# Performance work log

Hardware: AMD Instinct MI355X
Metric: run time of the kernel (lower is better)

## Reference

```python
import jax, jax.numpy as jnp
import numpy as np

B, N, T, S = 32, 102400, 64, 1600
PI = float(np.pi)
EPS = 1e-12  # numerical guard inside sqrt for cdist (diagonal is exactly 0)


def _cdist(a, b):
    # a: (..., P, 3), b: (..., Q, 3) -> (..., P, Q) euclidean distances
    sq = jnp.sum((a[..., :, None, :] - b[..., None, :, :]) ** 2, axis=-1)
    return jnp.sqrt(sq + EPS)


def _rigid_t(alpha, trans, sz, center):
    # alpha, trans: (B, T, 3). Returns XYZ (B,T,3,3), translation (B,T,3).
    c, s = jnp.cos(alpha), jnp.sin(alpha)
    z = jnp.zeros_like(c[..., 0]); o = jnp.ones_like(c[..., 0])
    X = jnp.stack([c[..., 0], -s[..., 0], z, s[..., 0], c[..., 0], z, z, z, o], -1).reshape(*alpha.shape[:2], 3, 3)
    Y = jnp.stack([c[..., 1], z, s[..., 1], z, o, z, -s[..., 1], z, c[..., 1]], -1).reshape(*alpha.shape[:2], 3, 3)
    Z = jnp.stack([o, z, z, z, c[..., 2], -s[..., 2], z, s[..., 2], c[..., 2]], -1).reshape(*alpha.shape[:2], 3, 3)
    XYZ = jnp.einsum('btij,btjk,btkl->btil', X, Y, Z)
    eye = jnp.eye(3, dtype=alpha.dtype)
    Tt = trans * sz[None, None, :] + jnp.einsum('m,btmk->btk', center, eye[None, None] - XYZ)
    return XYZ, Tt


def setup_inputs():
    key = jax.random.key(0)
    ks = jax.random.split(key, 6)
    x = jax.random.normal(ks[0], (B, 6, N), jnp.float32)
    w1 = jax.random.normal(ks[1], (3 * N, 32), jnp.float32) * 0.005
    b1 = jnp.zeros((32,), jnp.float32)
    w2 = jax.random.normal(ks[2], (32, 6 * T), jnp.float32) * 0.05
    b2 = jnp.zeros((6 * T,), jnp.float32)
    A = jax.random.normal(ks[3], (6, N), jnp.float32)
    mask = jax.random.uniform(ks[4], (T, T), jnp.float32)
    sz = jnp.array([128.0, 128.0, 64.0], jnp.float32)
    tess = jnp.arange(N, dtype=jnp.int32).reshape(T, S)  # equal-size partition
    return {'x': x, 'w1': w1, 'b1': b1, 'w2': w2, 'b2': b2, 'A': A, 'mask': mask, 'sz': sz, 'tess': tess}


def reference(x, w1, b1, w2, b2, A, mask, sz, tess):
    center = sz / 2.0
    # localization MLP on flattened xyz coords: (B, 3N) -> (B, T, 6)
    xflat = x[:, :3, :].reshape(B, 3 * N)
    h = jax.nn.relu(xflat @ w1 + b1)
    z_l = jnp.tanh(h @ w2 + b2).reshape(B, T, 6)
    # NOTE: original code uses z_l[:, :, 3:] for BOTH angles and translation
    r_, t_ = _rigid_t(PI * z_l[:, :, 3:], z_l[:, :, 3:], sz, center)
    x3 = x[:, :3, :]
    xg = x3[:, :, tess]  # gather: (B, 3, T, S)
    # out[b,j,p,n] = sum_k r_[b,p,k,j] * xg[b,k,p,n]  (matches einsum 'bkt,bkn->btn')
    rot = jnp.einsum('bpkj,bkpn->bjpn', r_, xg) + t_.transpose(0, 2, 1)[:, :, :, None]
    # scatter back into full point cloud (tess partitions N)
    X3 = jnp.zeros_like(x3).at[:, :, tess.reshape(-1)].set(rot.reshape(B, 3, N))
    X_t = jnp.concatenate([X3, x[:, 3:, :]], axis=1)  # colors pass through identity
    # regularizer on per-piece centroids
    pts_1 = A[:3][:, tess].mean(axis=2).T                 # (T, 3)
    pts_2 = X3[:, :, tess].mean(axis=3).transpose(0, 2, 1)  # (B, T, 3)
    diff = _cdist(pts_1, pts_1)[None] - _cdist(pts_2, pts_2)
    reg = jnp.sum((mask[None] * diff) ** 2, axis=(1, 2))  # (B,)
    return X_t, reg
```

## Files before the change

kernel.cpp:

```cpp
#include <hip/hip_runtime.h>
#include <hip/hip_bf16.h>
#include <math.h>

#define BB 32
#define NN 102400
#define TT 64
#define SS 1600
#define K3N (3 * NN)
#define KC 64
#define G1 512
#define NCHUNK (K3N / KC)
#define XP 68
#define WP 40
#define PI_F 3.14159265358979323846f

__global__ __launch_bounds__(256) void k1_gemm(const float* __restrict__ x,
                                               const float* __restrict__ w1,
                                               float* __restrict__ h_part) {
    __shared__ float xs[2][32 * XP];
    __shared__ float ws1[2][KC * WP];
    const int tid = threadIdx.x;
    const int ks = tid & 7;
    const int tile = tid >> 3;
    const int bg = tile & 7;
    const int cg = tile >> 3;
    const int sxb = tid >> 4, sxk = (tid & 15) * 4;
    const int swr = tid >> 3, swc = (tid & 7) * 4;

    float acc[4][8];
    #pragma unroll
    for (int j = 0; j < 4; ++j)
        #pragma unroll
        for (int c = 0; c < 8; ++c) acc[j][c] = 0.f;

    const int start = (int)(((long)blockIdx.x * NCHUNK) / G1);
    const int end   = (int)(((long)(blockIdx.x + 1) * NCHUNK) / G1);

    float4 rx0, rx1, rw0, rw1;
    {
        const int k0 = start * KC;
        rx0 = *(const float4*)(x + (size_t)sxb * 6 * NN + k0 + sxk);
        rx1 = *(const float4*)(x + (size_t)(sxb + 16) * 6 * NN + k0 + sxk);
        rw0 = *(const float4*)(w1 + (size_t)(k0 + swr) * 32 + swc);
        rw1 = *(const float4*)(w1 + (size_t)(k0 + swr + 32) * 32 + swc);
        *(float4*)(xs[0] + sxb * XP + sxk) = rx0;
        *(float4*)(xs[0] + (sxb + 16) * XP + sxk) = rx1;
        *(float4*)(ws1[0] + swr * WP + swc) = rw0;
        *(float4*)(ws1[0] + (swr + 32) * WP + swc) = rw1;
    }
    __syncthreads();

    int cur = 0;
    for (int chunk = start; chunk < end; ++chunk) {
        const bool more = (chunk + 1) < end;
        if (more) {
            const int k0 = (chunk + 1) * KC;
            rx0 = *(const float4*)(x + (size_t)sxb * 6 * NN + k0 + sxk);
            rx1 = *(const float4*)(x + (size_t)(sxb + 16) * 6 * NN + k0 + sxk);
            rw0 = *(const float4*)(w1 + (size_t)(k0 + swr) * 32 + swc);
            rw1 = *(const float4*)(w1 + (size_t)(k0 + swr + 32) * 32 + swc);
        }
        const float* xc = xs[cur];
        const float* wc = ws1[cur];
        #pragma unroll
        for (int i = 0; i < 8; ++i) {
            const int k = ks + 8 * i;
            const float4 wa = *(const float4*)(wc + k * WP + cg * 8);
            const float4 wb = *(const float4*)(wc + k * WP + cg * 8 + 4);
            float xv[4];
            #pragma unroll
            for (int j = 0; j < 4; ++j) xv[j] = xc[(bg + 8 * j) * XP + k];
            #pragma unroll
            for (int j = 0; j < 4; ++j) {
                acc[j][0] = fmaf(xv[j], wa.x, acc[j][0]);
                acc[j][1] = fmaf(xv[j], wa.y, acc[j][1]);
                acc[j][2] = fmaf(xv[j], wa.z, acc[j][2]);
                acc[j][3] = fmaf(xv[j], wa.w, acc[j][3]);
                acc[j][4] = fmaf(xv[j], wb.x, acc[j][4]);
                acc[j][5] = fmaf(xv[j], wb.y, acc[j][5]);
                acc[j][6] = fmaf(xv[j], wb.z, acc[j][6]);
                acc[j][7] = fmaf(xv[j], wb.w, acc[j][7]);
            }
        }
        if (more) {
            const int nb = cur ^ 1;
            *(float4*)(xs[nb] + sxb * XP + sxk) = rx0;
            *(float4*)(xs[nb] + (sxb + 16) * XP + sxk) = rx1;
            *(float4*)(ws1[nb] + swr * WP + swc) = rw0;
            *(float4*)(ws1[nb] + (swr + 32) * WP + swc) = rw1;
        }
        __syncthreads();
        cur ^= 1;
    }

    #pragma unroll
    for (int off = 1; off < 8; off <<= 1) {
        #pragma unroll
        for (int j = 0; j < 4; ++j)
            #pragma unroll
            for (int c = 0; c < 8; ++c)
                acc[j][c] += __shfl_xor(acc[j][c], off, 64);
    }
    if (ks == 0) {
        float* hp = h_part + (size_t)blockIdx.x * 1024;
        #pragma unroll
        for (int j = 0; j < 4; ++j) {
            const int b = bg + 8 * j;
            #pragma unroll
            for (int c = 0; c < 8; ++c)
                hp[b * 32 + cg * 8 + c] = acc[j][c];
        }
    }
}

__global__ __launch_bounds__(256) void kb_fused(const float* __restrict__ h_part,
                                                const float* __restrict__ b1,
                                                const float* __restrict__ w2,
                                                const float* __restrict__ b2,
                                                const float* __restrict__ sz,
                                                const float* __restrict__ A,
                                                const int* __restrict__ tess,
                                                float* __restrict__ RT,
                                                float* __restrict__ pts1) {
    const int blk = blockIdx.x;
    if (blk < BB) {
        const int bb = blk;
        __shared__ float part[8][32];
        __shared__ float hsh[32];
        const int c = threadIdx.x & 31, g = threadIdx.x >> 5;
        float s = 0.f;
        for (int j = g; j < G1; j += 8) s += h_part[(size_t)j * 1024 + bb * 32 + c];
        part[g][c] = s;
        __syncthreads();
        if (threadIdx.x < 32) {
            float acc = 0.f;
            #pragma unroll
            for (int g2 = 0; g2 < 8; ++g2) acc += part[g2][threadIdx.x];
            hsh[threadIdx.x] = fmaxf(acc + b1[threadIdx.x], 0.f);
        }
        __syncthreads();
        const int t = threadIdx.x;
        if (t < TT) {
            float z[3];
            #pragma unroll
            for (int j = 0; j < 3; ++j) {
                const int col = 6 * t + 3 + j;
                float s2 = b2[col];
                #pragma unroll 8
                for (int cc = 0; cc < 32; ++cc) s2 = fmaf(hsh[cc], w2[cc * 384 + col], s2);
                z[j] = tanhf(s2);
            }
            float c0, s0, c1, s1, c2, s2v;
            sincosf(PI_F * z[0], &s0, &c0);
            sincosf(PI_F * z[1], &s1, &c1);
            sincosf(PI_F * z[2], &s2v, &c2);
            const float R00 = c0 * c1;
            const float R01 = -s0 * c2 + c0 * s1 * s2v;
            const float R02 = s0 * s2v + c0 * s1 * c2;
            const float R10 = s0 * c1;
            const float R11 = c0 * c2 + s0 * s1 * s2v;
            const float R12 = -c0 * s2v + s0 * s1 * c2;
            const float R20 = -s1;
            const float R21 = c1 * s2v;
            const float R22 = c1 * c2;
            const float szx = sz[0], szy = sz[1], szz = sz[2];
            const float cx = 0.5f * szx, cy = 0.5f * szy, cz = 0.5f * szz;
            const float T0 = z[0] * szx + cx - (cx * R00 + cy * R10 + cz * R20);
            const float T1 = z[1] * szy + cy - (cx * R01 + cy * R11 + cz * R21);
            const float T2 = z[2] * szz + cz - (cx * R02 + cy * R12 + cz * R22);
            float* o = RT + (bb * TT + t) * 12;
            o[0] = R00; o[1] = R10; o[2]  = R20; o[3]  = T0;
            o[4] = R01; o[5] = R11; o[6]  = R21; o[7]  = T1;
            o[8] = R02; o[9] = R12; o[10] = R22; o[11] = T2;
        }
    } else {
        const int t = blk - BB;
        const int* tr = tess + t * SS;
        float s0 = 0.f, s1 = 0.f, s2 = 0.f;
        for (int s = threadIdx.x; s < SS; s += 256) {
            const int idx = tr[s];
            s0 += A[idx]; s1 += A[NN + idx]; s2 += A[2 * NN + idx];
        }
        #pragma unroll
        for (int o = 32; o > 0; o >>= 1) {
            s0 += __shfl_down(s0, o, 64);
            s1 += __shfl_down(s1, o, 64);
            s2 += __shfl_down(s2, o, 64);
        }
        __shared__ float red[4 * 3];
        const int lane = threadIdx.x & 63, wv = threadIdx.x >> 6;
        if (lane == 0) { red[wv * 3] = s0; red[wv * 3 + 1] = s1; red[wv * 3 + 2] = s2; }
        __syncthreads();
        if (threadIdx.x < 3) {
            const float s = red[threadIdx.x] + red[3 + threadIdx.x] + red[6 + threadIdx.x] + red[9 + threadIdx.x];
            pts1[t * 3 + threadIdx.x] = s * (1.0f / SS);
        }
    }
}

__global__ __launch_bounds__(256) void k3_transform(const float* __restrict__ x,
                                                    const int* __restrict__ tess,
                                                    const float* __restrict__ RT,
                                                    float* __restrict__ out,
                                                    float* __restrict__ pts2) {
    const int blk = blockIdx.x;
    const int b = blk / TT, t = blk % TT;
    const float* p = RT + blk * 12;
    const float M00 = p[0], M01 = p[1], M02 = p[2], T0 = p[3];
    const float M10 = p[4], M11 = p[5], M12 = p[6], T1 = p[7];
    const float M20 = p[8], M21 = p[9], M22 = p[10], T2 = p[11];
    const float* xb = x + (size_t)b * 6 * NN;
    float* ob = out + (size_t)b * 6 * NN;
    const int* tr = tess + t * SS;
    float s0 = 0.f, s1 = 0.f, s2 = 0.f;
    for (int s = threadIdx.x; s < SS; s += 256) {
        const int idx = tr[s];
        const float x0 = xb[idx], x1 = xb[NN + idx], x2 = xb[2 * NN + idx];
        const float y0 = fmaf(M00, x0, fmaf(M01, x1, fmaf(M02, x2, T0)));
        const float y1 = fmaf(M10, x0, fmaf(M11, x1, fmaf(M12, x2, T1)));
        const float y2 = fmaf(M20, x0, fmaf(M21, x1, fmaf(M22, x2, T2)));
        ob[idx] = y0; ob[NN + idx] = y1; ob[2 * NN + idx] = y2;
        s0 += y0; s1 += y1; s2 += y2;
    }
    const int n0 = t * SS;
    for (int i = threadIdx.x; i < 1200; i += 256) {
        const int ch = i / 400, r = i - ch * 400;
        const size_t off = (size_t)(3 + ch) * NN + n0 + r * 4;
        *(float4*)(ob + off) = *(const float4*)(xb + off);
    }
    #pragma unroll
    for (int o = 32; o > 0; o >>= 1) {
        s0 += __shfl_down(s0, o, 64);
        s1 += __shfl_down(s1, o, 64);
        s2 += __shfl_down(s2, o, 64);
    }
    __shared__ float red[4 * 3];
    const int lane = threadIdx.x & 63, wv = threadIdx.x >> 6;
    if (lane == 0) { red[wv * 3] = s0; red[wv * 3 + 1] = s1; red[wv * 3 + 2] = s2; }
    __syncthreads();
    if (threadIdx.x < 3) {
        const float s = red[threadIdx.x] + red[3 + threadIdx.x] + red[6 + threadIdx.x] + red[9 + threadIdx.x];
        pts2[blk * 3 + threadIdx.x] = s * (1.0f / SS);
    }
}

__global__ __launch_bounds__(256) void k5_reg(const float* __restrict__ pts1,
                                              const float* __restrict__ pts2,
                                              const float* __restrict__ mask,
                                              float* __restrict__ out) {
    const int b = blockIdx.x;
    __shared__ float p1[TT * 3], p2[TT * 3];
    for (int i = threadIdx.x; i < TT * 3; i += 256) {
        p1[i] = pts1[i];
        p2[i] = pts2[b * TT * 3 + i];
    }
    __syncthreads();
    float acc = 0.f;
    for (int pr = threadIdx.x; pr < TT * TT; pr += 256) {
        const int t = pr >> 6, u = pr & 63;
        float dx = p1[t * 3] - p1[u * 3];
        float dy = p1[t * 3 + 1] - p1[u * 3 + 1];
        float dz = p1[t * 3 + 2] - p1[u * 3 + 2];
        const float d1 = sqrtf(dx * dx + dy * dy + dz * dz + 1e-12f);
        dx = p2[t * 3] - p2[u * 3];
        dy = p2[t * 3 + 1] - p2[u * 3 + 1];
        dz = p2[t * 3 + 2] - p2[u * 3 + 2];
        const float d2 = sqrtf(dx * dx + dy * dy + dz * dz + 1e-12f);
        const float d = mask[pr] * (d1 - d2);
        acc = fmaf(d, d, acc);
    }
    #pragma unroll
    for (int o = 32; o > 0; o >>= 1) acc += __shfl_down(acc, o, 64);
    __shared__ float red[4];
    const int lane = threadIdx.x & 63, wv = threadIdx.x >> 6;
    if (lane == 0) red[wv] = acc;
    __syncthreads();
    if (threadIdx.x == 0) {
        out[(size_t)BB * 6 * NN + b] = red[0] + red[1] + red[2] + red[3];
    }
}

extern "C" void kernel_launch(void* const* d_in, const int* in_sizes, int n_in,
                              void* d_out, int out_size, void* d_ws, size_t ws_size,
                              hipStream_t stream) {
    const float* x    = (const float*)d_in[0];
    const float* w1   = (const float*)d_in[1];
    const float* b1   = (const float*)d_in[2];
    const float* w2   = (const float*)d_in[3];
    const float* b2   = (const float*)d_in[4];
    const float* A    = (const float*)d_in[5];
    const float* mask = (const float*)d_in[6];
    const float* sz   = (const float*)d_in[7];
    const int*   tess = (const int*)d_in[8];
    float* out = (float*)d_out;
    float* ws  = (float*)d_ws;

    float* h_part = ws;
    float* RT     = h_part + (size_t)G1 * 1024;
    float* pts2   = RT + BB * TT * 12;
    float* pts1   = pts2 + BB * TT * 3;

    k1_gemm<<<G1, 256, 0, stream>>>(x, w1, h_part);
    kb_fused<<<BB + TT, 256, 0, stream>>>(h_part, b1, w2, b2, sz, A, tess, RT, pts1);
    k3_transform<<<BB * TT, 256, 0, stream>>>(x, tess, RT, out, pts2);
    k5_reg<<<BB, 256, 0, stream>>>(pts1, pts2, mask, out);
}
```

Before: 76.77 us.

## Restructure split-K GEMM thread mapping with float4 LDS reads and more blocks

The first GEMM kernel now gives each wave its own contiguous 8-wide K slice and reads x from shared memory as float4 vectors. The cross-lane shuffle reduction is replaced by one shuffle plus a shared-memory reduction across waves. The grid size becomes a runtime value, defaulting to 1024 blocks and capped by workspace size, with launch bounds requesting 4 blocks per CU. This is meant to cut LDS instruction count and shuffle overhead and to raise parallelism. In exchange the second kernel must reduce twice as many partial sums.

```diff
diff --git a/kernel.cpp b/kernel.cpp
--- a/kernel.cpp
+++ b/kernel.cpp
@@ -8,20 +8,20 @@
 #define SS 1600
 #define K3N (3 * NN)
 #define KC 64
-#define G1 512
 #define NCHUNK (K3N / KC)
 #define XP 68
 #define WP 40
 #define PI_F 3.14159265358979323846f
 
-__global__ __launch_bounds__(256) void k1_gemm(const float* __restrict__ x,
-                                               const float* __restrict__ w1,
-                                               float* __restrict__ h_part) {
+__global__ __launch_bounds__(256, 4) void k1_gemm(const float* __restrict__ x,
+                                                  const float* __restrict__ w1,
+                                                  float* __restrict__ h_part,
+                                                  int g1) {
     __shared__ float xs[2][32 * XP];
     __shared__ float ws1[2][KC * WP];
     const int tid = threadIdx.x;
-    const int ks = tid & 7;
-    const int tile = tid >> 3;
+    const int ks = tid >> 5;
+    const int tile = tid & 31;
     const int bg = tile & 7;
     const int cg = tile >> 3;
     const int sxb = tid >> 4, sxk = (tid & 15) * 4;
@@ -33,8 +33,8 @@
         #pragma unroll
         for (int c = 0; c < 8; ++c) acc[j][c] = 0.f;
 
-    const int start = (int)(((long)blockIdx.x * NCHUNK) / G1);
-    const int end   = (int)(((long)(blockIdx.x + 1) * NCHUNK) / G1);
+    const int start = (int)(((long)blockIdx.x * NCHUNK) / g1);
+    const int end   = (int)(((long)(blockIdx.x + 1) * NCHUNK) / g1);
 
     float4 rx0, rx1, rw0, rw1;
     {
@@ -63,23 +63,28 @@
         const float* xc = xs[cur];
         const float* wc = ws1[cur];
         #pragma unroll
-        for (int i = 0; i < 8; ++i) {
-            const int k = ks + 8 * i;
-            const float4 wa = *(const float4*)(wc + k * WP + cg * 8);
-            const float4 wb = *(const float4*)(wc + k * WP + cg * 8 + 4);
-            float xv[4];
-            #pragma unroll
-            for (int j = 0; j < 4; ++j) xv[j] = xc[(bg + 8 * j) * XP + k];
-            #pragma unroll
-            for (int j = 0; j < 4; ++j) {
-                acc[j][0] = fmaf(xv[j], wa.x, acc[j][0]);
-                acc[j][1] = fmaf(xv[j], wa.y, acc[j][1]);
-                acc[j][2] = fmaf(xv[j], wa.z, acc[j][2]);
-                acc[j][3] = fmaf(xv[j], wa.w, acc[j][3]);
-                acc[j][4] = fmaf(xv[j], wb.x, acc[j][4]);
-                acc[j][5] = fmaf(xv[j], wb.y, acc[j][5]);
-                acc[j][6] = fmaf(xv[j], wb.z, acc[j][6]);
-                acc[j][7] = fmaf(xv[j], wb.w, acc[j][7]);
+        for (int i = 0; i < 2; ++i) {
+            const int kb0 = ks * 8 + i * 4;
+            float4 xv[4];
+            #pragma unroll
+            for (int j = 0; j < 4; ++j)
+                xv[j] = *(const float4*)(xc + (bg + 8 * j) * XP + kb0);
+            #pragma unroll
+            for (int kk = 0; kk < 4; ++kk) {
+                const float4 wa = *(const float4*)(wc + (kb0 + kk) * WP + cg * 8);
+                const float4 wb = *(const float4*)(wc + (kb0 + kk) * WP + cg * 8 + 4);
+                #pragma unroll
+                for (int j = 0; j < 4; ++j) {
+                    const float xj = kk == 0 ? xv[j].x : (kk == 1 ? xv[j].y : (kk == 2 ? xv[j].z : xv[j].w));
+                    acc[j][0] = fmaf(xj, wa.x, acc[j][0]);
+                    acc[j][1] = fmaf(xj, wa.y, acc[j][1]);
+                    acc[j][2] = fmaf(xj, wa.z, acc[j][2]);
+                    acc[j][3] = fmaf(xj, wa.w, acc[j][3]);
+                    acc[j][4] = fmaf(xj, wb.x, acc[j][4]);
+                    acc[j][5] = fmaf(xj, wb.y, acc[j][5]);
+                    acc[j][6] = fmaf(xj, wb.z, acc[j][6]);
+                    acc[j][7] = fmaf(xj, wb.w, acc[j][7]);
+                }
             }
         }
         if (more) {
@@ -94,21 +99,44 @@
     }
 
     #pragma unroll
-    for (int off = 1; off < 8; off <<= 1) {
-        #pragma unroll
-        for (int j = 0; j < 4; ++j)
-            #pragma unroll
-            for (int c = 0; c < 8; ++c)
-                acc[j][c] += __shfl_xor(acc[j][c], off, 64);
-    }
-    if (ks == 0) {
+    for (int j = 0; j < 4; ++j)
+        #pragma unroll
+        for (int c = 0; c < 8; ++c)
+            acc[j][c] += __shfl_xor(acc[j][c], 32, 64);
+
+    float* red = &xs[0][0];
+    const int wv = tid >> 6, lane = tid & 63;
+    if (wv > 0 && lane < 32) {
+        float* dst = red + (wv - 1) * 1152 + tile * 36;
+        #pragma unroll
+        for (int j = 0; j < 4; ++j) {
+            float4 v0; v0.x = acc[j][0]; v0.y = acc[j][1]; v0.z = acc[j][2]; v0.w = acc[j][3];
+            float4 v1; v1.x = acc[j][4]; v1.y = acc[j][5]; v1.z = acc[j][6]; v1.w = acc[j][7];
+            *(float4*)(dst + j * 8) = v0;
+            *(float4*)(dst + j * 8 + 4) = v1;
+        }
+    }
+    __syncthreads();
+    if (wv == 0 && lane < 32) {
+        #pragma unroll
+        for (int w2 = 0; w2 < 3; ++w2) {
+            const float* srcp = red + w2 * 1152 + tile * 36;
+            #pragma unroll
+            for (int j = 0; j < 4; ++j) {
+                const float4 v0 = *(const float4*)(srcp + j * 8);
+                const float4 v1 = *(const float4*)(srcp + j * 8 + 4);
+                acc[j][0] += v0.x; acc[j][1] += v0.y; acc[j][2] += v0.z; acc[j][3] += v0.w;
+                acc[j][4] += v1.x; acc[j][5] += v1.y; acc[j][6] += v1.z; acc[j][7] += v1.w;
+            }
+        }
         float* hp = h_part + (size_t)blockIdx.x * 1024;
         #pragma unroll
         for (int j = 0; j < 4; ++j) {
-            const int b = bg + 8 * j;
-            #pragma unroll
-            for (int c = 0; c < 8; ++c)
-                hp[b * 32 + cg * 8 + c] = acc[j][c];
+            float4 v0; v0.x = acc[j][0]; v0.y = acc[j][1]; v0.z = acc[j][2]; v0.w = acc[j][3];
+            float4 v1; v1.x = acc[j][4]; v1.y = acc[j][5]; v1.z = acc[j][6]; v1.w = acc[j][7];
+            float* dst = hp + (bg + 8 * j) * 32 + cg * 8;
+            *(float4*)(dst) = v0;
+            *(float4*)(dst + 4) = v1;
         }
     }
 }
@@ -121,7 +149,8 @@
                                                 const float* __restrict__ A,
                                                 const int* __restrict__ tess,
                                                 float* __restrict__ RT,
-                                                float* __restrict__ pts1) {
+                                                float* __restrict__ pts1,
+                                                int g1) {
     const int blk = blockIdx.x;
     if (blk < BB) {
         const int bb = blk;
@@ -129,7 +158,7 @@
         __shared__ float hsh[32];
         const int c = threadIdx.x & 31, g = threadIdx.x >> 5;
         float s = 0.f;
-        for (int j = g; j < G1; j += 8) s += h_part[(size_t)j * 1024 + bb * 32 + c];
+        for (int j = g; j < g1; j += 8) s += h_part[(size_t)j * 1024 + bb * 32 + c];
         part[g][c] = s;
         __syncthreads();
         if (threadIdx.x < 32) {
@@ -295,13 +324,16 @@
     float* out = (float*)d_out;
     float* ws  = (float*)d_ws;
 
+    int g1 = 1024;
+    while ((size_t)((size_t)g1 * 1024 + 2048 * 12 + 2048 * 3 + 192) * 4 > ws_size && g1 > 128) g1 >>= 1;
+
     float* h_part = ws;
-    float* RT     = h_part + (size_t)G1 * 1024;
+    float* RT     = h_part + (size_t)g1 * 1024;
     float* pts2   = RT + BB * TT * 12;
     float* pts1   = pts2 + BB * TT * 3;
 
-    k1_gemm<<<G1, 256, 0, stream>>>(x, w1, h_part);
-    kb_fused<<<BB + TT, 256, 0, stream>>>(h_part, b1, w2, b2, sz, A, tess, RT, pts1);
+    k1_gemm<<<g1, 256, 0, stream>>>(x, w1, h_part, g1);
+    kb_fused<<<BB + TT, 256, 0, stream>>>(h_part, b1, w2, b2, sz, A, tess, RT, pts1, g1);
     k3_transform<<<BB * TT, 256, 0, stream>>>(x, tess, RT, out, pts2);
     k5_reg<<<BB, 256, 0, stream>>>(pts1, pts2, mask, out);
 }
```

Measured after the change: 140.1 us. +82.5%, slower.

## Overlap color passthrough copy and centroid reduction with the GEMM kernel

Applied to the files above, without the earlier changes.

Extra blocks are added to the first-layer GEMM launch: one group copies the color channels from input to output, and another computes the reference centroids pts1. Both jobs move out of the later kernels, so the bandwidth-bound copy runs while the GEMM reads x and w1 and no longer sits on the dependent transform path. The rigid-transform kernel now only builds rotations. Both jobs now compete with the GEMM for bandwidth, and the copy becomes a grid-stride loop instead of per-tile copies.

```diff
diff --git a/kernel.cpp b/kernel.cpp
--- a/kernel.cpp
+++ b/kernel.cpp
@@ -9,192 +9,201 @@
 #define K3N (3 * NN)
 #define KC 64
 #define G1 512
+#define CPB 512
 #define NCHUNK (K3N / KC)
 #define XP 68
 #define WP 40
 #define PI_F 3.14159265358979323846f
 
-__global__ __launch_bounds__(256) void k1_gemm(const float* __restrict__ x,
+__global__ __launch_bounds__(256) void k1_mega(const float* __restrict__ x,
                                                const float* __restrict__ w1,
-                                               float* __restrict__ h_part) {
-    __shared__ float xs[2][32 * XP];
-    __shared__ float ws1[2][KC * WP];
+                                               const float* __restrict__ A,
+                                               const int* __restrict__ tess,
+                                               float* __restrict__ h_part,
+                                               float* __restrict__ out,
+                                               float* __restrict__ pts1) {
     const int tid = threadIdx.x;
-    const int ks = tid & 7;
-    const int tile = tid >> 3;
-    const int bg = tile & 7;
-    const int cg = tile >> 3;
-    const int sxb = tid >> 4, sxk = (tid & 15) * 4;
-    const int swr = tid >> 3, swc = (tid & 7) * 4;
-
-    float acc[4][8];
-    #pragma unroll
-    for (int j = 0; j < 4; ++j)
-        #pragma unroll
-        for (int c = 0; c < 8; ++c) acc[j][c] = 0.f;
-
-    const int start = (int)(((long)blockIdx.x * NCHUNK) / G1);
-    const int end   = (int)(((long)(blockIdx.x + 1) * NCHUNK) / G1);
-
-    float4 rx0, rx1, rw0, rw1;
-    {
-        const int k0 = start * KC;
-        rx0 = *(const float4*)(x + (size_t)sxb * 6 * NN + k0 + sxk);
-        rx1 = *(const float4*)(x + (size_t)(sxb + 16) * 6 * NN + k0 + sxk);
-        rw0 = *(const float4*)(w1 + (size_t)(k0 + swr) * 32 + swc);
-        rw1 = *(const float4*)(w1 + (size_t)(k0 + swr + 32) * 32 + swc);
-        *(float4*)(xs[0] + sxb * XP + sxk) = rx0;
-        *(float4*)(xs[0] + (sxb + 16) * XP + sxk) = rx1;
-        *(float4*)(ws1[0] + swr * WP + swc) = rw0;
-        *(float4*)(ws1[0] + (swr + 32) * WP + swc) = rw1;
-    }
-    __syncthreads();
-
-    int cur = 0;
-    for (int chunk = start; chunk < end; ++chunk) {
-        const bool more = (chunk + 1) < end;
-        if (more) {
-            const int k0 = (chunk + 1) * KC;
+    if (blockIdx.x < G1) {
+        __shared__ float xs[2][32 * XP];
+        __shared__ float ws1[2][KC * WP];
+        const int ks = tid & 7;
+        const int tile = tid >> 3;
+        const int bg = tile & 7;
+        const int cg = tile >> 3;
+        const int sxb = tid >> 4, sxk = (tid & 15) * 4;
+        const int swr = tid >> 3, swc = (tid & 7) * 4;
+
+        float acc[4][8];
+        #pragma unroll
+        for (int j = 0; j < 4; ++j)
+            #pragma unroll
+            for (int c = 0; c < 8; ++c) acc[j][c] = 0.f;
+
+        const int start = (int)(((long)blockIdx.x * NCHUNK) / G1);
+        const int end   = (int)(((long)(blockIdx.x + 1) * NCHUNK) / G1);
+
+        float4 rx0, rx1, rw0, rw1;
+        {
+            const int k0 = start * KC;
             rx0 = *(const float4*)(x + (size_t)sxb * 6 * NN + k0 + sxk);
             rx1 = *(const float4*)(x + (size_t)(sxb + 16) * 6 * NN + k0 + sxk);
             rw0 = *(const float4*)(w1 + (size_t)(k0 + swr) * 32 + swc);
             rw1 = *(const float4*)(w1 + (size_t)(k0 + swr + 32) * 32 + swc);
-        }
-        const float* xc = xs[cur];
-        const float* wc = ws1[cur];
-        #pragma unroll
-        for (int i = 0; i < 8; ++i) {
-            const int k = ks + 8 * i;
-            const float4 wa = *(const float4*)(wc + k * WP + cg * 8);
-            const float4 wb = *(const float4*)(wc + k * WP + cg * 8 + 4);
-            float xv[4];
+            *(float4*)(xs[0] + sxb * XP + sxk) = rx0;
+            *(float4*)(xs[0] + (sxb + 16) * XP + sxk) = rx1;
+            *(float4*)(ws1[0] + swr * WP + swc) = rw0;
+            *(float4*)(ws1[0] + (swr + 32) * WP + swc) = rw1;
+        }
+        __syncthreads();
+
+        int cur = 0;
+        for (int chunk = start; chunk < end; ++chunk) {
+            const bool more = (chunk + 1) < end;
+            if (more) {
+                const int k0 = (chunk + 1) * KC;
+                rx0 = *(const float4*)(x + (size_t)sxb * 6 * NN + k0 + sxk);
+                rx1 = *(const float4*)(x + (size_t)(sxb + 16) * 6 * NN + k0 + sxk);
+                rw0 = *(const float4*)(w1 + (size_t)(k0 + swr) * 32 + swc);
+                rw1 = *(const float4*)(w1 + (size_t)(k0 + swr + 32) * 32 + swc);
+            }
+            const float* xc = xs[cur];
+            const float* wc = ws1[cur];
             #pragma unroll
-            for (int j = 0; j < 4; ++j) xv[j] = xc[(bg + 8 * j) * XP + k];
+            for (int i = 0; i < 8; ++i) {
+                const int k = ks + 8 * i;
+                const float4 wa = *(const float4*)(wc + k * WP + cg * 8);
+                const float4 wb = *(const float4*)(wc + k * WP + cg * 8 + 4);
+                float xv[4];
+                #pragma unroll
+                for (int j = 0; j < 4; ++j) xv[j] = xc[(bg + 8 * j) * XP + k];
+                #pragma unroll
+                for (int j = 0; j < 4; ++j) {
+                    acc[j][0] = fmaf(xv[j], wa.x, acc[j][0]);
+                    acc[j][1] = fmaf(xv[j], wa.y, acc[j][1]);
+                    acc[j][2] = fmaf(xv[j], wa.z, acc[j][2]);
+                    acc[j][3] = fmaf(xv[j], wa.w, acc[j][3]);
+                    acc[j][4] = fmaf(xv[j], wb.x, acc[j][4]);
+                    acc[j][5] = fmaf(xv[j], wb.y, acc[j][5]);
+                    acc[j][6] = fmaf(xv[j], wb.z, acc[j][6]);
+                    acc[j][7] = fmaf(xv[j], wb.w, acc[j][7]);
+                }
+            }
+            if (more) {
+                const int nb = cur ^ 1;
+                *(float4*)(xs[nb] + sxb * XP + sxk) = rx0;
+                *(float4*)(xs[nb] + (sxb + 16) * XP + sxk) = rx1;
+                *(float4*)(ws1[nb] + swr * WP + swc) = rw0;
+                *(float4*)(ws1[nb] + (swr + 32) * WP + swc) = rw1;
+            }
+            __syncthreads();
+            cur ^= 1;
+        }
+
+        #pragma unroll
+        for (int off = 1; off < 8; off <<= 1) {
+            #pragma unroll
+            for (int j = 0; j < 4; ++j)
+                #pragma unroll
+                for (int c = 0; c < 8; ++c)
+                    acc[j][c] += __shfl_xor(acc[j][c], off, 64);
+        }
+        if (ks == 0) {
+            float* hp = h_part + (size_t)blockIdx.x * 1024;
             #pragma unroll
             for (int j = 0; j < 4; ++j) {
-                acc[j][0] = fmaf(xv[j], wa.x, acc[j][0]);
-                acc[j][1] = fmaf(xv[j], wa.y, acc[j][1]);
-                acc[j][2] = fmaf(xv[j], wa.z, acc[j][2]);
-                acc[j][3] = fmaf(xv[j], wa.w, acc[j][3]);
-                acc[j][4] = fmaf(xv[j], wb.x, acc[j][4]);
-                acc[j][5] = fmaf(xv[j], wb.y, acc[j][5]);
-                acc[j][6] = fmaf(xv[j], wb.z, acc[j][6]);
-                acc[j][7] = fmaf(xv[j], wb.w, acc[j][7]);
+                const int b = bg + 8 * j;
+                #pragma unroll
+                for (int c = 0; c < 8; ++c)
+                    hp[b * 32 + cg * 8 + c] = acc[j][c];
             }
         }
-        if (more) {
-            const int nb = cur ^ 1;
-            *(float4*)(xs[nb] + sxb * XP + sxk) = rx0;
-            *(float4*)(xs[nb] + (sxb + 16) * XP + sxk) = rx1;
-            *(float4*)(ws1[nb] + swr * WP + swc) = rw0;
-            *(float4*)(ws1[nb] + (swr + 32) * WP + swc) = rw1;
-        }
+    } else if (blockIdx.x < G1 + CPB) {
+        const int cb = blockIdx.x - G1;
+        for (long i = (long)cb * 256 + tid; i < 2457600L; i += (long)CPB * 256) {
+            const int b = (int)(i / 76800);
+            const int rem = (int)(i - (long)b * 76800);
+            const size_t off = (size_t)b * (6 * NN) + K3N + (size_t)rem * 4;
+            *(float4*)(out + off) = *(const float4*)(x + off);
+        }
+    } else {
+        const int t = blockIdx.x - G1 - CPB;
+        const int* tr = tess + t * SS;
+        float s0 = 0.f, s1 = 0.f, s2 = 0.f;
+        for (int s = tid; s < SS; s += 256) {
+            const int idx = tr[s];
+            s0 += A[idx]; s1 += A[NN + idx]; s2 += A[2 * NN + idx];
+        }
+        #pragma unroll
+        for (int o = 32; o > 0; o >>= 1) {
+            s0 += __shfl_down(s0, o, 64);
+            s1 += __shfl_down(s1, o, 64);
+            s2 += __shfl_down(s2, o, 64);
+        }
+        __shared__ float red[4 * 3];
+        const int lane = tid & 63, wv = tid >> 6;
+        if (lane == 0) { red[wv * 3] = s0; red[wv * 3 + 1] = s1; red[wv * 3 + 2] = s2; }
         __syncthreads();
-        cur ^= 1;
-    }
-
-    #pragma unroll
-    for (int off = 1; off < 8; off <<= 1) {
-        #pragma unroll
-        for (int j = 0; j < 4; ++j)
-            #pragma unroll
-            for (int c = 0; c < 8; ++c)
-                acc[j][c] += __shfl_xor(acc[j][c], off, 64);
-    }
-    if (ks == 0) {
-        float* hp = h_part + (size_t)blockIdx.x * 1024;
-        #pragma unroll
-        for (int j = 0; j < 4; ++j) {
-            const int b = bg + 8 * j;
-            #pragma unroll
-            for (int c = 0; c < 8; ++c)
-                hp[b * 32 + cg * 8 + c] = acc[j][c];
-        }
-    }
-}
-
-__global__ __launch_bounds__(256) void kb_fused(const float* __restrict__ h_part,
+        if (tid < 3) {
+            const float s = red[tid] + red[3 + tid] + red[6 + tid] + red[9 + tid];
+            pts1[t * 3 + tid] = s * (1.0f / SS);
+        }
+    }
+}
+
+__global__ __launch_bounds__(256) void kb_rigid(const float* __restrict__ h_part,
                                                 const float* __restrict__ b1,
                                                 const float* __restrict__ w2,
                                                 const float* __restrict__ b2,
                                                 const float* __restrict__ sz,
-                                                const float* __restrict__ A,
-                                                const int* __restrict__ tess,
-                                                float* __restrict__ RT,
-                                                float* __restrict__ pts1) {
-    const int blk = blockIdx.x;
-    if (blk < BB) {
-        const int bb = blk;
-        __shared__ float part[8][32];
-        __shared__ float hsh[32];
-        const int c = threadIdx.x & 31, g = threadIdx.x >> 5;
-        float s = 0.f;
-        for (int j = g; j < G1; j += 8) s += h_part[(size_t)j * 1024 + bb * 32 + c];
-        part[g][c] = s;
-        __syncthreads();
-        if (threadIdx.x < 32) {
-            float acc = 0.f;
-            #pragma unroll
-            for (int g2 = 0; g2 < 8; ++g2) acc += part[g2][threadIdx.x];
-            hsh[threadIdx.x] = fmaxf(acc + b1[threadIdx.x], 0.f);
-        }
-        __syncthreads();
-        const int t = threadIdx.x;
-        if (t < TT) {
-            float z[3];
-            #pragma unroll
-            for (int j = 0; j < 3; ++j) {
-                const int col = 6 * t + 3 + j;
-                float s2 = b2[col];
-                #pragma unroll 8
-                for (int cc = 0; cc < 32; ++cc) s2 = fmaf(hsh[cc], w2[cc * 384 + col], s2);
-                z[j] = tanhf(s2);
-            }
-            float c0, s0, c1, s1, c2, s2v;
-            sincosf(PI_F * z[0], &s0, &c0);
-            sincosf(PI_F * z[1], &s1, &c1);
-            sincosf(PI_F * z[2], &s2v, &c2);
-            const float R00 = c0 * c1;
-            const float R01 = -s0 * c2 + c0 * s1 * s2v;
-            const float R02 = s0 * s2v + c0 * s1 * c2;
-            const float R10 = s0 * c1;
-            const float R11 = c0 * c2 + s0 * s1 * s2v;
-            const float R12 = -c0 * s2v + s0 * s1 * c2;
-            const float R20 = -s1;
-            const float R21 = c1 * s2v;
-            const float R22 = c1 * c2;
-            const float szx = sz[0], szy = sz[1], szz = sz[2];
-            const float cx = 0.5f * szx, cy = 0.5f * szy, cz = 0.5f * szz;
-            const float T0 = z[0] * szx + cx - (cx * R00 + cy * R10 + cz * R20);
-            const float T1 = z[1] * szy + cy - (cx * R01 + cy * R11 + cz * R21);
-            const float T2 = z[2] * szz + cz - (cx * R02 + cy * R12 + cz * R22);
-            float* o = RT + (bb * TT + t) * 12;
-            o[0] = R00; o[1] = R10; o[2]  = R20; o[3]  = T0;
-            o[4] = R01; o[5] = R11; o[6]  = R21; o[7]  = T1;
-            o[8] = R02; o[9] = R12; o[10] = R22; o[11] = T2;
-        }
-    } else {
-        const int t = blk - BB;
-        const int* tr = tess + t * SS;
-        float s0 = 0.f, s1 = 0.f, s2 = 0.f;
-        for (int s = threadIdx.x; s < SS; s += 256) {
-            const int idx = tr[s];
-            s0 += A[idx]; s1 += A[NN + idx]; s2 += A[2 * NN + idx];
-        }
-        #pragma unroll
-        for (int o = 32; o > 0; o >>= 1) {
-            s0 += __shfl_down(s0, o, 64);
-            s1 += __shfl_down(s1, o, 64);
-            s2 += __shfl_down(s2, o, 64);
-        }
-        __shared__ float red[4 * 3];
-        const int lane = threadIdx.x & 63, wv = threadIdx.x >> 6;
-        if (lane == 0) { red[wv * 3] = s0; red[wv * 3 + 1] = s1; red[wv * 3 + 2] = s2; }
-        __syncthreads();
-        if (threadIdx.x < 3) {
-            const float s = red[threadIdx.x] + red[3 + threadIdx.x] + red[6 + threadIdx.x] + red[9 + threadIdx.x];
-            pts1[t * 3 + threadIdx.x] = s * (1.0f / SS);
-        }
+                                                float* __restrict__ RT) {
+    const int bb = blockIdx.x;
+    __shared__ float part[8][32];
+    __shared__ float hsh[32];
+    const int c = threadIdx.x & 31, g = threadIdx.x >> 5;
+    float s = 0.f;
+    for (int j = g; j < G1; j += 8) s += h_part[(size_t)j * 1024 + bb * 32 + c];
+    part[g][c] = s;
+    __syncthreads();
+    if (threadIdx.x < 32) {
+        float acc = 0.f;
+        #pragma unroll
+        for (int g2 = 0; g2 < 8; ++g2) acc += part[g2][threadIdx.x];
+        hsh[threadIdx.x] = fmaxf(acc + b1[threadIdx.x], 0.f);
+    }
+    __syncthreads();
+    const int t = threadIdx.x;
+    if (t < TT) {
+        float z[3];
+        #pragma unroll
+        for (int j = 0; j < 3; ++j) {
+            const int col = 6 * t + 3 + j;
+            float s2 = b2[col];
+            #pragma unroll 8
+            for (int cc = 0; cc < 32; ++cc) s2 = fmaf(hsh[cc], w2[cc * 384 + col], s2);
+            z[j] = tanhf(s2);
+        }
+        float c0, s0, c1, s1, c2, s2v;
+        sincosf(PI_F * z[0], &s0, &c0);
+        sincosf(PI_F * z[1], &s1, &c1);
+        sincosf(PI_F * z[2], &s2v, &c2);
+        const float R00 = c0 * c1;
+        const float R01 = -s0 * c2 + c0 * s1 * s2v;
+        const float R02 = s0 * s2v + c0 * s1 * c2;
+        const float R10 = s0 * c1;
+        const float R11 = c0 * c2 + s0 * s1 * s2v;
+        const float R12 = -c0 * s2v + s0 * s1 * c2;
+        const float R20 = -s1;
+        const float R21 = c1 * s2v;
+        const float R22 = c1 * c2;
+        const float szx = sz[0], szy = sz[1], szz = sz[2];
+        const float cx = 0.5f * szx, cy = 0.5f * szy, cz = 0.5f * szz;
+        const float T0 = z[0] * szx + cx - (cx * R00 + cy * R10 + cz * R20);
+        const float T1 = z[1] * szy + cy - (cx * R01 + cy * R11 + cz * R21);
+        const float T2 = z[2] * szz + cz - (cx * R02 + cy * R12 + cz * R22);
+        float* o = RT + (bb * TT + t) * 12;
+        o[0] = R00; o[1] = R10; o[2]  = R20; o[3]  = T0;
+        o[4] = R01; o[5] = R11; o[6]  = R21; o[7]  = T1;
+        o[8] = R02; o[9] = R12; o[10] = R22; o[11] = T2;
     }
 }
 
@@ -222,12 +231,6 @@
         ob[idx] = y0; ob[NN + idx] = y1; ob[2 * NN + idx] = y2;
         s0 += y0; s1 += y1; s2 += y2;
     }
-    const int n0 = t * SS;
-    for (int i = threadIdx.x; i < 1200; i += 256) {
-        const int ch = i / 400, r = i - ch * 400;
-        const size_t off = (size_t)(3 + ch) * NN + n0 + r * 4;
-        *(float4*)(ob + off) = *(const float4*)(xb + off);
-    }
     #pragma unroll
     for (int o = 32; o > 0; o >>= 1) {
         s0 += __shfl_down(s0, o, 64);
@@ -300,8 +303,8 @@
     float* pts2   = RT + BB * TT * 12;
     float* pts1   = pts2 + BB * TT * 3;
 
-    k1_gemm<<<G1, 256, 0, stream>>>(x, w1, h_part);
-    kb_fused<<<BB + TT, 256, 0, stream>>>(h_part, b1, w2, b2, sz, A, tess, RT, pts1);
+    k1_mega<<<G1 + CPB + TT, 256, 0, stream>>>(x, w1, A, tess, h_part, out, pts1);
+    kb_rigid<<<BB, 256, 0, stream>>>(h_part, b1, w2, b2, sz, RT);
     k3_transform<<<BB * TT, 256, 0, stream>>>(x, tess, RT, out, pts2);
     k5_reg<<<BB, 256, 0, stream>>>(pts1, pts2, mask, out);
 }
```

Result: faster. 74.64 us (-2.8%).

## Load GEMM tiles via direct global-to-LDS and fold color copy into GEMM

Applied to the files above, without the earlier changes.

The split-K GEMM kernel now stages x and w1 tiles with direct global-to-LDS loads, using a doubled K chunk and XOR-swizzled LDS layouts in place of padded ones. The pass-through copy of the color channels moves out of the transform kernel and is spread across the GEMM chunks, so those loads and stores overlap the FMA work. The aim is to hide the memory-bound copy behind a compute loop that is also memory-bound, and to cut register staging. In exchange the GEMM loop carries extra loads, address arithmetic and stores, which adds register pressure and memory traffic.

```diff
diff --git a/kernel.cpp b/kernel.cpp
--- a/kernel.cpp
+++ b/kernel.cpp
@@ -7,25 +7,41 @@
 #define TT 64
 #define SS 1600
 #define K3N (3 * NN)
-#define KC 64
+#define KC 128
 #define G1 512
-#define NCHUNK (K3N / KC)
-#define XP 68
-#define WP 40
+#define NCH (K3N / KC)
+#define HI_F4 2457600
+#define F4B (HI_F4 / G1)
 #define PI_F 3.14159265358979323846f
 
-__global__ __launch_bounds__(256) void k1_gemm(const float* __restrict__ x,
+#define AS1 __attribute__((address_space(1)))
+#define AS3 __attribute__((address_space(3)))
+
+__device__ __forceinline__ void gload16(const float* g, float* l) {
+    __builtin_amdgcn_global_load_lds((const AS1 void*)g, (AS3 void*)l, 16, 0, 0);
+}
+
+__global__ __launch_bounds__(256) void k1_mega(const float* __restrict__ x,
                                                const float* __restrict__ w1,
-                                               float* __restrict__ h_part) {
-    __shared__ float xs[2][32 * XP];
-    __shared__ float ws1[2][KC * WP];
+                                               float* __restrict__ h_part,
+                                               float* __restrict__ out) {
+    __shared__ float xs[2][32 * KC];
+    __shared__ float wls[2][KC * 32];
     const int tid = threadIdx.x;
+    const int lane = tid & 63, wv = tid >> 6;
     const int ks = tid & 7;
-    const int tile = tid >> 3;
-    const int bg = tile & 7;
-    const int cg = tile >> 3;
-    const int sxb = tid >> 4, sxk = (tid & 15) * 4;
-    const int swr = tid >> 3, swc = (tid & 7) * 4;
+    const int bg = (tid >> 3) & 7;
+    const int cg = wv;
+
+    size_t gx[4], gw[4];
+    #pragma unroll
+    for (int n = 0; n < 4; ++n) {
+        const int s = n * 256 + tid;
+        const int b = s >> 5, q = s & 31;
+        gx[n] = (size_t)b * 6 * NN + ((4 * (q - b)) & 127);
+        const int k = s >> 3, p = s & 7;
+        gw[n] = (size_t)k * 32 + (((p >> 1) ^ (k & 3)) * 8 + (p & 1) * 4);
+    }
 
     float acc[4][8];
     #pragma unroll
@@ -33,43 +49,60 @@
         #pragma unroll
         for (int c = 0; c < 8; ++c) acc[j][c] = 0.f;
 
-    const int start = (int)(((long)blockIdx.x * NCHUNK) / G1);
-    const int end   = (int)(((long)(blockIdx.x + 1) * NCHUNK) / G1);
-
-    float4 rx0, rx1, rw0, rw1;
+    const int start = (int)(((long)blockIdx.x * NCH) / G1);
+    const int end   = (int)(((long)(blockIdx.x + 1) * NCH) / G1);
+    const int nch   = end - start;
+    const int quota = (F4B + nch - 1) / nch;
+    const int cbase = blockIdx.x * F4B;
+
     {
         const int k0 = start * KC;
-        rx0 = *(const float4*)(x + (size_t)sxb * 6 * NN + k0 + sxk);
-        rx1 = *(const float4*)(x + (size_t)(sxb + 16) * 6 * NN + k0 + sxk);
-        rw0 = *(const float4*)(w1 + (size_t)(k0 + swr) * 32 + swc);
-        rw1 = *(const float4*)(w1 + (size_t)(k0 + swr + 32) * 32 + swc);
-        *(float4*)(xs[0] + sxb * XP + sxk) = rx0;
-        *(float4*)(xs[0] + (sxb + 16) * XP + sxk) = rx1;
-        *(float4*)(ws1[0] + swr * WP + swc) = rw0;
-        *(float4*)(ws1[0] + (swr + 32) * WP + swc) = rw1;
+        #pragma unroll
+        for (int n = 0; n < 4; ++n) {
+            gload16(x + gx[n] + k0, &xs[0][n * 1024 + wv * 256]);
+            gload16(w1 + gw[n] + (size_t)k0 * 32, &wls[0][n * 1024 + wv * 256]);
+        }
     }
     __syncthreads();
 
     int cur = 0;
     for (int chunk = start; chunk < end; ++chunk) {
-        const bool more = (chunk + 1) < end;
-        if (more) {
+        const int ci = chunk - start;
+        if (chunk + 1 < end) {
             const int k0 = (chunk + 1) * KC;
-            rx0 = *(const float4*)(x + (size_t)sxb * 6 * NN + k0 + sxk);
-            rx1 = *(const float4*)(x + (size_t)(sxb + 16) * 6 * NN + k0 + sxk);
-            rw0 = *(const float4*)(w1 + (size_t)(k0 + swr) * 32 + swc);
-            rw1 = *(const float4*)(w1 + (size_t)(k0 + swr + 32) * 32 + swc);
+            const int nb = cur ^ 1;
+            #pragma unroll
+            for (int n = 0; n < 4; ++n) {
+                gload16(x + gx[n] + k0, &xs[nb][n * 1024 + wv * 256]);
+                gload16(w1 + gw[n] + (size_t)k0 * 32, &wls[nb][n * 1024 + wv * 256]);
+            }
+        }
+        float4 cv[5]; size_t coff[5]; bool cp[5];
+        #pragma unroll
+        for (int r = 0; r < 5; ++r) {
+            const int v = r * 256 + tid;
+            const int u = ci * quota + v;
+            cp[r] = (v < quota) && (u < F4B);
+            const int g = cbase + (cp[r] ? u : 0);
+            const int b2 = g / 76800;
+            const int rem = g - b2 * 76800;
+            coff[r] = (size_t)b2 * 6 * NN + K3N + (size_t)rem * 4;
+            cv[r] = *(const float4*)(x + coff[r]);
         }
         const float* xc = xs[cur];
-        const float* wc = ws1[cur];
-        #pragma unroll
-        for (int i = 0; i < 8; ++i) {
+        const float* wc = wls[cur];
+        #pragma unroll
+        for (int i = 0; i < 16; ++i) {
             const int k = ks + 8 * i;
-            const float4 wa = *(const float4*)(wc + k * WP + cg * 8);
-            const float4 wb = *(const float4*)(wc + k * WP + cg * 8 + 4);
             float xv[4];
             #pragma unroll
-            for (int j = 0; j < 4; ++j) xv[j] = xc[(bg + 8 * j) * XP + k];
+            for (int j = 0; j < 4; ++j) {
+                const int b = bg + 8 * j;
+                xv[j] = xc[b * KC + ((k + 4 * b) & (KC - 1))];
+            }
+            const int wo = k * 32 + ((cg ^ (k & 3)) * 8);
+            const float4 wa = *(const float4*)(wc + wo);
+            const float4 wb = *(const float4*)(wc + wo + 4);
             #pragma unroll
             for (int j = 0; j < 4; ++j) {
                 acc[j][0] = fmaf(xv[j], wa.x, acc[j][0]);
@@ -82,13 +115,9 @@
                 acc[j][7] = fmaf(xv[j], wb.w, acc[j][7]);
             }
         }
-        if (more) {
-            const int nb = cur ^ 1;
-            *(float4*)(xs[nb] + sxb * XP + sxk) = rx0;
-            *(float4*)(xs[nb] + (sxb + 16) * XP + sxk) = rx1;
-            *(float4*)(ws1[nb] + swr * WP + swc) = rw0;
-            *(float4*)(ws1[nb] + (swr + 32) * WP + swc) = rw1;
-        }
+        #pragma unroll
+        for (int r = 0; r < 5; ++r)
+            if (cp[r]) *(float4*)(out + coff[r]) = cv[r];
         __syncthreads();
         cur ^= 1;
     }
@@ -222,12 +251,6 @@
         ob[idx] = y0; ob[NN + idx] = y1; ob[2 * NN + idx] = y2;
         s0 += y0; s1 += y1; s2 += y2;
     }
-    const int n0 = t * SS;
-    for (int i = threadIdx.x; i < 1200; i += 256) {
-        const int ch = i / 400, r = i - ch * 400;
-        const size_t off = (size_t)(3 + ch) * NN + n0 + r * 4;
-        *(float4*)(ob + off) = *(const float4*)(xb + off);
-    }
     #pragma unroll
     for (int o = 32; o > 0; o >>= 1) {
         s0 += __shfl_down(s0, o, 64);
@@ -300,7 +323,7 @@
     float* pts2   = RT + BB * TT * 12;
     float* pts1   = pts2 + BB * TT * 3;
 
-    k1_gemm<<<G1, 256, 0, stream>>>(x, w1, h_part);
+    k1_mega<<<G1, 256, 0, stream>>>(x, w1, h_part, out);
     kb_fused<<<BB + TT, 256, 0, stream>>>(h_part, b1, w2, b2, sz, A, tess, RT, pts1);
     k3_transform<<<BB * TT, 256, 0, stream>>>(x, tess, RT, out, pts2);
     k5_reg<<<BB, 256, 0, stream>>>(pts1, pts2, mask, out);
```

Result: slower. 88.06 us (+14.7%).
